# Performance work log

Measured on AMD Instinct MI355X. Metric: run time of the kernel, lower is better.

Reference implementation:

```python
import jax, jax.numpy as jnp
import numpy as np

B, N, IN_C, OUT_C, H, M, E = 1, 20000, 256, 64, 4, 30, 320000
EPS = 1e-6


def _projection_matrix(m, d, seed=0):
    # NodeFormer create_projection_matrix: stacked transposed-QR blocks, rows
    # rescaled by norms of iid gaussian rows (scaling=0).
    rng = np.random.RandomState(seed)
    blocks = []
    nb_full = m // d
    for _ in range(nb_full):
        q, _ = np.linalg.qr(rng.randn(d, d))
        blocks.append(q.T)
    rem = m - nb_full * d
    if rem > 0:
        q, _ = np.linalg.qr(rng.randn(d, d))
        blocks.append(q.T[:rem])
    final = np.vstack(blocks)
    multiplier = np.linalg.norm(rng.randn(m, d), axis=1)
    return jnp.asarray(multiplier[:, None] * final, dtype=jnp.float32)


def _linear(key, out_f, in_f):
    k1, k2 = jax.random.split(key)
    s = 1.0 / np.sqrt(in_f)
    w = jax.random.uniform(k1, (out_f, in_f), jnp.float32, -s, s)
    b = jax.random.uniform(k2, (out_f,), jnp.float32, -s, s)
    return w, b


def setup_inputs() -> dict:
    key = jax.random.key(0)
    ks = jax.random.split(key, 8)
    Wq_w, Wq_b = _linear(ks[3], H * OUT_C, IN_C)
    Wk_w, Wk_b = _linear(ks[4], H * OUT_C, IN_C)
    Wv_w, Wv_b = _linear(ks[5], H * OUT_C, IN_C)
    Wo_w, Wo_b = _linear(ks[6], OUT_C, H * OUT_C)
    return {
        'z': jax.random.normal(ks[0], (B, N, IN_C), jnp.float32),
        'feat': jax.random.normal(ks[1], (B, N, IN_C), jnp.float32),
        'edge_index': jax.random.randint(ks[2], (2, E), 0, N),
        'tau': jnp.asarray(0.25, jnp.float32),
        'Wq_w': Wq_w, 'Wq_b': Wq_b,
        'Wk_w': Wk_w, 'Wk_b': Wk_b,
        'Wv_w': Wv_w, 'Wv_b': Wv_b,
        'Wo_w': Wo_w, 'Wo_b': Wo_b,
        'b_param': jnp.full((1, H), 0.1, jnp.float32),  # rb_order=1, sigmoid init
        'proj': _projection_matrix(M, OUT_C),
    }


def _softmax_kernel(x, proj, is_query):
    # Performer positive softmax kernel feature map. x: [B,N,H,D] -> [B,N,H,M]
    d = x.shape[-1]
    x = x * (float(d) ** -0.25)
    ratio = 1.0 / jnp.sqrt(jnp.asarray(proj.shape[0], x.dtype))
    xd = jnp.einsum('bnhd,md->bnhm', x, proj)
    diag = 0.5 * jnp.sum(x * x, axis=-1, keepdims=True)
    if is_query:
        mx = jnp.max(xd, axis=-1, keepdims=True)
    else:
        mx = jnp.max(jnp.max(xd, axis=-1, keepdims=True), axis=1, keepdims=True)
    return ratio * (jnp.exp(xd - diag - mx) + EPS)


def reference(z, feat, edge_index, tau, Wq_w, Wq_b, Wk_w, Wk_b, Wv_w, Wv_b,
              Wo_w, Wo_b, b_param, proj):
    Bn, Nn = z.shape[0], z.shape[1]
    q = (feat @ Wq_w.T + Wq_b).reshape(Bn, Nn, H, OUT_C)
    k = (feat @ Wk_w.T + Wk_b).reshape(Bn, Nn, H, OUT_C)
    v = (z @ Wv_w.T + Wv_b).reshape(Bn, Nn, H, OUT_C)

    inv = 1.0 / jnp.sqrt(tau)
    qp = _softmax_kernel(q * inv, proj, True)    # [B,N,H,M]
    kp = _softmax_kernel(k * inv, proj, False)   # [B,N,H,M]

    # Linear (kernelized) attention, O(N*H*M*D)
    kvs = jnp.einsum('bnhm,bnhd->bhmd', kp, v)
    num = jnp.einsum('bnhm,bhmd->bnhd', qp, kvs)
    den = jnp.einsum('bnhm,bhm->bnh', qp, jnp.sum(kp, axis=1))[..., None]
    z_next = num / den                            # [B,N,H,D]

    # Relational bias: GCN-style normalized scatter with per-head scalar weight
    row, col = edge_index[0], edge_index[1]
    d_in = jnp.zeros((Nn,), z.dtype).at[col].add(1.0)
    d_out = jnp.zeros((Nn,), z.dtype).at[row].add(1.0)
    edge_w = jnp.nan_to_num(jnp.sqrt(1.0 / d_in[col]) * jnp.sqrt(1.0 / d_out[row]),
                            nan=0.0, posinf=0.0, neginf=0.0)    # [E]
    msgs = v[:, row] * edge_w[None, :, None, None]              # [B,E,H,D]
    agg = jnp.zeros_like(v).at[:, col].add(msgs)                # [B,N,H,D]
    z_next = z_next + jax.nn.sigmoid(b_param[0])[None, None, :, None] * agg

    out = z_next.reshape(Bn, Nn, H * OUT_C) @ Wo_w.T + Wo_b     # [B,N,OUT_C]
    return out
```

## Files before the change

kernel.cpp:

```cpp
#include <hip/hip_runtime.h>

#define NN 20000
#define EE 320000
#define RATIO_F 0.18257418583505536f
#define EPS_F 1e-6f
#define SCALE_D4 0.35355339059327373f
#define NCH 157

typedef _Float16 f16x8 __attribute__((ext_vector_type(8)));
typedef _Float16 f16x4 __attribute__((ext_vector_type(4)));
typedef float f32x4 __attribute__((ext_vector_type(4)));

__device__ __forceinline__ unsigned fenc(float x) {
  unsigned u = __float_as_uint(x);
  return (u & 0x80000000u) ? ~u : (u | 0x80000000u);
}
__device__ __forceinline__ float fdec(unsigned u) {
  return (u & 0x80000000u) ? __uint_as_float(u & 0x7FFFFFFFu) : __uint_as_float(~u);
}
__device__ __forceinline__ void fma4(float* a, float s, float4 b) {
  a[0] = fmaf(s, b.x, a[0]);
  a[1] = fmaf(s, b.y, a[1]);
  a[2] = fmaf(s, b.z, a[2]);
  a[3] = fmaf(s, b.w, a[3]);
}
__device__ __forceinline__ void gload16(const void* g, void* l) {
  __builtin_amdgcn_global_load_lds(
      (const __attribute__((address_space(1))) unsigned int*)g,
      (__attribute__((address_space(3))) unsigned int*)l, 16, 0, 0);
}

__global__ __launch_bounds__(256)
void k0_build(const float* __restrict__ Wq, const float* __restrict__ Wk,
              const float* __restrict__ Wv, const float* __restrict__ bq,
              const float* __restrict__ bk, const float* __restrict__ bv,
              const float* __restrict__ proj, const float* __restrict__ tau,
              const float* __restrict__ Wo, const int* __restrict__ ei,
              const float* __restrict__ feat, const float* __restrict__ zin,
              _Float16* __restrict__ Wf, float* __restrict__ bbig,
              _Float16* __restrict__ WoFh, _Float16* __restrict__ WoFl,
              int* __restrict__ dini, int* __restrict__ douti,
              _Float16* __restrict__ feath, _Float16* __restrict__ zh16) {
  const int blk = blockIdx.x;
  const int i = threadIdx.x;
  if (blk >= 1401) {
    int cb = blk - 1401;
    const float* src;
    _Float16* dst;
    if (cb < 2500) { src = feat; dst = feath; }
    else           { src = zin;  dst = zh16; cb -= 2500; }
    const size_t off = (size_t)cb * 2048 + i * 8;
    const float4 a = *(const float4*)(src + off);
    const float4 b = *(const float4*)(src + off + 4);
    f16x8 o;
    o[0] = (_Float16)a.x; o[1] = (_Float16)a.y;
    o[2] = (_Float16)a.z; o[3] = (_Float16)a.w;
    o[4] = (_Float16)b.x; o[5] = (_Float16)b.y;
    o[6] = (_Float16)b.z; o[7] = (_Float16)b.w;
    *(f16x8*)(dst + off) = o;
    return;
  }
  if (blk >= 1088) {
    const int q = (blk - 1088) * 256 + i;
    if (q < EE / 4) {
      const int4 r4 = *(const int4*)(ei + q * 4);
      const int4 c4 = *(const int4*)(ei + EE + q * 4);
      atomicAdd(&dini[c4.x], 1); atomicAdd(&dini[c4.y], 1);
      atomicAdd(&dini[c4.z], 1); atomicAdd(&dini[c4.w], 1);
      atomicAdd(&douti[r4.x], 1); atomicAdd(&douti[r4.y], 1);
      atomicAdd(&douti[r4.z], 1); atomicAdd(&douti[r4.w], 1);
    }
    return;
  }
  const int kt = i >> 5, gg = (i >> 3) & 3, j = i & 7;
  if (blk >= 1024) {
    const int col = blk - 1024;
    const float val = Wo[col * 256 + i];
    const int lane = gg * 16 + (col & 15);
    const size_t off = (size_t)((col >> 4) * 8 + kt) * 512 + lane * 8 + j;
    const _Float16 hb = (_Float16)val;
    WoFh[off] = hb;
    WoFl[off] = (_Float16)(val - (float)hb);
    return;
  }
  const int col = blk;
  const float s = rsqrtf(tau[0]) * SCALE_D4;
  float val = 0.f, bias = 0.f;
  if (col < 256) {
    val = Wq[col * 256 + i]; bias = bq[col];
  } else if (col < 512) {
    const int c = col - 256;
    val = Wk[c * 256 + i]; bias = bk[c];
  } else if (col < 768) {
    const int c = col - 512;
    val = Wv[c * 256 + i]; bias = bv[c];
  } else {
    const int rr = col - 768;
    const int grp = rr >> 7;
    const int h = (rr >> 5) & 3, m = rr & 31;
    if (m < 30) {
      const float* W = grp ? Wk : Wq;
      const float* bb = grp ? bk : bq;
      float a = 0.f, ba = 0.f;
#pragma unroll 8
      for (int d = 0; d < 64; ++d) {
        const float pr = proj[m * 64 + d];
        a  = fmaf(pr, W[(h * 64 + d) * 256 + i], a);
        ba = fmaf(pr, bb[h * 64 + d], ba);
      }
      val = s * a; bias = s * ba;
    }
  }
  const int lane = gg * 16 + (col & 15);
  const size_t off = (size_t)((col >> 4) * 8 + kt) * 512 + lane * 8 + j;
  Wf[off] = (_Float16)val;
  if (i == 0) bbig[col] = bias;
}

__device__ __forceinline__ int ct_of(int s, int isv, int h, int y) {
  if (isv) return 32 + (y - 4) * 8 + s;
  if (s < 4)  return h * 4 + s;
  if (s < 8)  return 16 + h * 4 + (s - 4);
  if (s < 10) return 48 + 2 * h + (s - 8);
  return 56 + 2 * h + (s - 10);
}

__global__ __launch_bounds__(512, 4)
void k1m(const _Float16* __restrict__ feath, const _Float16* __restrict__ zh16,
         const _Float16* __restrict__ Wf, const float* __restrict__ bbig,
         const float* __restrict__ tau,
         _Float16* __restrict__ qph, _Float16* __restrict__ kbufh,
         _Float16* __restrict__ vh, unsigned* __restrict__ kmaxU,
         const int* __restrict__ ei, const int* __restrict__ coff,
         int* __restrict__ cursor, int* __restrict__ crow,
         const int* __restrict__ douti, float* __restrict__ rw) {
  __shared__ __align__(16) _Float16 blds[12 * 2048];
  const int blk = blockIdx.x;
  const int t = threadIdx.x;
  if (blk >= 1567) {
    const int n = (blk - 1567) * 512 + t;
    if (n < NN) rw[n] = rsqrtf((float)douti[n]);
    return;
  }
  if (blk >= 942) {
    const int e = (blk - 942) * 512 + t;
    const int r = ei[e], c = ei[EE + e];
    const int pos = atomicAdd(&cursor[c], 1);
    crow[coff[c] + pos] = r;
    return;
  }
  const int y = blk / 157;
  const int h = y & 3;
  const int wid = t >> 6, lane = t & 63;
  const int g = lane >> 4, cl = lane & 15;
  const int rbase = (blk - y * 157) * 128 + wid * 16;
  int arow = rbase + cl; if (arow > NN - 1) arow = NN - 1;

  if (y < 4) {
    const _Float16* arp = feath + (size_t)arow * 256;
#pragma unroll
    for (int r = 0; r < 6; ++r) {
      const int idx = r * 4096 + t * 8;
      const int s = idx >> 11, wi = idx & 2047;
      gload16(Wf + (size_t)ct_of(s, 0, h, y) * 4096 + wi, &blds[idx]);
    }
    f16x8 Ah[4];
#pragma unroll
    for (int l = 0; l < 4; ++l)
      Ah[l] = *(const f16x8*)(arp + l * 32 + g * 8);
    __syncthreads();
    f16x8 Ah2[4];
#pragma unroll
    for (int l = 0; l < 4; ++l)
      Ah2[l] = *(const f16x8*)(arp + (l + 4) * 32 + g * 8);
    f32x4 acc[12];
#pragma unroll
    for (int s = 0; s < 12; ++s) acc[s] = (f32x4){0.f, 0.f, 0.f, 0.f};
#pragma unroll
    for (int ktl = 0; ktl < 4; ++ktl) {
#pragma unroll
      for (int s = 0; s < 12; ++s) {
        const f16x8 b = *(const f16x8*)&blds[s * 2048 + ktl * 512 + lane * 8];
        acc[s] = __builtin_amdgcn_mfma_f32_16x16x32_f16(Ah[ktl], b, acc[s], 0, 0, 0);
      }
    }
    __syncthreads();
#pragma unroll
    for (int r = 0; r < 6; ++r) {
      const int idx = r * 4096 + t * 8;
      const int s = idx >> 11, wi = idx & 2047;
      gload16(Wf + (size_t)ct_of(s, 0, h, y) * 4096 + 2048 + wi, &blds[idx]);
    }
    __syncthreads();
#pragma unroll
    for (int ktl = 0; ktl < 4; ++ktl) {
#pragma unroll
      for (int s = 0; s < 12; ++s) {
        const f16x8 b = *(const f16x8*)&blds[s * 2048 + ktl * 512 + lane * 8];
        acc[s] = __builtin_amdgcn_mfma_f32_16x16x32_f16(Ah2[ktl], b, acc[s], 0, 0, 0);
      }
    }
#pragma unroll
    for (int s = 0; s < 12; ++s) {
      const float bb = bbig[ct_of(s, 0, h, y) * 16 + cl];
#pragma unroll
      for (int j = 0; j < 4; ++j) acc[s][j] += bb;
    }
    const float sc = rsqrtf(tau[0]) * SCALE_D4;
    const float h2 = 0.5f * sc * sc;
    float dsq[4], dsk[4];
#pragma unroll
    for (int j = 0; j < 4; ++j) {
      dsq[j] = acc[0][j] * acc[0][j] + acc[1][j] * acc[1][j] +
               acc[2][j] * acc[2][j] + acc[3][j] * acc[3][j];
      dsk[j] = acc[4][j] * acc[4][j] + acc[5][j] * acc[5][j] +
               acc[6][j] * acc[6][j] + acc[7][j] * acc[7][j];
    }
#pragma unroll
    for (int m = 1; m < 16; m <<= 1) {
#pragma unroll
      for (int j = 0; j < 4; ++j) {
        dsq[j] += __shfl_xor(dsq[j], m);
        dsk[j] += __shfl_xor(dsk[j], m);
      }
    }
    {
#pragma unroll
      for (int j = 0; j < 4; ++j) {
        const float x0 = acc[8][j], x1 = acc[9][j];
        float mv = fmaxf(x0, (cl < 14) ? x1 : -3.4e38f);
#pragma unroll
        for (int m = 1; m < 16; m <<= 1) mv = fmaxf(mv, __shfl_xor(mv, m));
        const float dg = h2 * dsq[j];
        const int r = rbase + 4 * g + j;
        if (r < NN) {
          _Float16* dst = qph + (size_t)r * 120 + h * 30;
          dst[cl] = (_Float16)(RATIO_F * (expf(x0 - dg - mv) + EPS_F));
          if (cl < 14)
            dst[16 + cl] = (_Float16)(RATIO_F * (expf(x1 - dg - mv) + EPS_F));
        }
      }
    }
    {
      float wmax = -3.4e38f;
#pragma unroll
      for (int j = 0; j < 4; ++j) {
        const float x0 = acc[10][j], x1 = acc[11][j];
        float mv = fmaxf(x0, (cl < 14) ? x1 : -3.4e38f);
#pragma unroll
        for (int m = 1; m < 16; m <<= 1) mv = fmaxf(mv, __shfl_xor(mv, m));
        wmax = fmaxf(wmax, mv);
        const float dg = h2 * dsk[j];
        const int r = rbase + 4 * g + j;
        if (r < NN) {
          _Float16* dst = kbufh + (size_t)r * 120 + h * 30;
          dst[cl] = (_Float16)(x0 - dg);
          if (cl < 14) dst[16 + cl] = (_Float16)(x1 - dg);
        }
      }
      wmax = fmaxf(wmax, __shfl_xor(wmax, 16));
      wmax = fmaxf(wmax, __shfl_xor(wmax, 32));
      if (lane == 0) atomicMax(&kmaxU[h], fenc(wmax));
    }
  } else {
    const _Float16* arp = zh16 + (size_t)arow * 256;
#pragma unroll
    for (int r = 0; r < 4; ++r) {
      const int idx = r * 4096 + t * 8;
      const int s = idx >> 11, wi = idx & 2047;
      gload16(Wf + (size_t)ct_of(s, 1, h, y) * 4096 + wi, &blds[idx]);
    }
    f16x8 Ah[4];
#pragma unroll
    for (int l = 0; l < 4; ++l)
      Ah[l] = *(const f16x8*)(arp + l * 32 + g * 8);
    __syncthreads();
    f16x8 Ah2[4];
#pragma unroll
    for (int l = 0; l < 4; ++l)
      Ah2[l] = *(const f16x8*)(arp + (l + 4) * 32 + g * 8);
    f32x4 acc[8];
#pragma unroll
    for (int s = 0; s < 8; ++s) acc[s] = (f32x4){0.f, 0.f, 0.f, 0.f};
#pragma unroll
    for (int ktl = 0; ktl < 4; ++ktl) {
#pragma unroll
      for (int s = 0; s < 8; ++s) {
        const f16x8 b = *(const f16x8*)&blds[s * 2048 + ktl * 512 + lane * 8];
        acc[s] = __builtin_amdgcn_mfma_f32_16x16x32_f16(Ah[ktl], b, acc[s], 0, 0, 0);
      }
    }
    __syncthreads();
#pragma unroll
    for (int r = 0; r < 4; ++r) {
      const int idx = r * 4096 + t * 8;
      const int s = idx >> 11, wi = idx & 2047;
      gload16(Wf + (size_t)ct_of(s, 1, h, y) * 4096 + 2048 + wi, &blds[idx]);
    }
    __syncthreads();
#pragma unroll
    for (int ktl = 0; ktl < 4; ++ktl) {
#pragma unroll
      for (int s = 0; s < 8; ++s) {
        const f16x8 b = *(const f16x8*)&blds[s * 2048 + ktl * 512 + lane * 8];
        acc[s] = __builtin_amdgcn_mfma_f32_16x16x32_f16(Ah2[ktl], b, acc[s], 0, 0, 0);
      }
    }
#pragma unroll
    for (int s = 0; s < 8; ++s) {
      const int ct = ct_of(s, 1, h, y);
      const float bb = bbig[ct * 16 + cl];
      const int colb = (ct - 32) * 16 + cl;
#pragma unroll
      for (int j = 0; j < 4; ++j) {
        const int r = rbase + 4 * g + j;
        if (r < NN) vh[(size_t)r * 256 + colb] = (_Float16)(acc[s][j] + bb);
      }
    }
  }
}

__global__ __launch_bounds__(256)
void k3_kvs(const _Float16* __restrict__ kbr, const _Float16* __restrict__ vh,
            const unsigned* __restrict__ kmaxU, float* __restrict__ partial) {
  __shared__ float kpch[128 * 32];
  __shared__ float vch[128 * 68];
  const int h = blockIdx.y;
  const int n0 = blockIdx.x * 128;
  const int cnt = min(128, NN - n0);
  const int t = threadIdx.x;
  const float mx = fdec(kmaxU[h]);
  const int m = t >> 3, dg = t & 7, d0 = dg * 8;
#pragma unroll
  for (int l = 0; l < 15; ++l) {
    const int flat = l * 256 + t;
    const int nl = flat / 30, mm = flat - nl * 30;
    kpch[nl * 32 + mm] = (nl < cnt)
        ? RATIO_F * (expf((float)kbr[(size_t)(n0 + nl) * 120 + h * 30 + mm] - mx) + EPS_F)
        : 0.f;
  }
#pragma unroll
  for (int l = 0; l < 8; ++l) {
    const int f4 = l * 256 + t;
    const int nl = f4 >> 4, dd = (f4 & 15) * 4;
    float4 vv = make_float4(0.f, 0.f, 0.f, 0.f);
    if (nl < cnt) {
      f16x4 u = *(const f16x4*)(vh + (size_t)(n0 + nl) * 256 + h * 64 + dd);
      vv = make_float4((float)u[0], (float)u[1], (float)u[2], (float)u[3]);
    }
    *(float4*)&vch[nl * 68 + dd] = vv;
  }
  __syncthreads();
  float acc[8] = {0, 0, 0, 0, 0, 0, 0, 0};
  float asum = 0.f;
  const int ms = (m < 30) ? m : 0;
  for (int nl = 0; nl < cnt; ++nl) {
    const float kv = kpch[nl * 32 + ms];
    const float4 va = *(const float4*)&vch[nl * 68 + d0];
    const float4 vb = *(const float4*)&vch[nl * 68 + d0 + 4];
    fma4(&acc[0], kv, va);
    fma4(&acc[4], kv, vb);
    asum += kv;
  }
  if (m < 30) {
    float* dst = partial + ((size_t)blockIdx.y * NCH + blockIdx.x) * 1952 + m * 64 + d0;
#pragma unroll
    for (int j = 0; j < 8; ++j) dst[j] = acc[j];
    if (dg == 0)
      partial[((size_t)blockIdx.y * NCH + blockIdx.x) * 1952 + 1920 + m] = asum;
  }
}

__global__ __launch_bounds__(256)
void k7g3b(const int* __restrict__ coff, const int* __restrict__ crow,
           const float* __restrict__ rw, const _Float16* __restrict__ vh,
           _Float16* __restrict__ aggh, const float* __restrict__ partial,
           float* __restrict__ kvs, float* __restrict__ ksum) {
  const int blk = blockIdx.x;
  if (blk >= 5000) {
    const int idx = (blk - 5000) * 256 + threadIdx.x;
    if (idx >= 4 * 1952) return;
    const int h = idx / 1952, q = idx - h * 1952;
    float s = 0.f;
    for (int c = 0; c < NCH; ++c)
      s += partial[((size_t)h * NCH + c) * 1952 + q];
    if (q < 1920) kvs[h * 1920 + q] = s;
    else if (q < 1950) ksum[h * 30 + (q - 1920)] = s;
    return;
  }
  const int node = blk * 4 + (threadIdx.x >> 6);
  const int lane = threadIdx.x & 63;
  const int o0 = coff[node], o1 = coff[node + 1];
  float a0 = 0.f, a1 = 0.f, a2 = 0.f, a3 = 0.f;
  if (o1 > o0) {
    int e = o0;
    for (; e + 16 <= o1; e += 16) {
      int rr[16];
#pragma unroll
      for (int u = 0; u < 16; ++u) rr[u] = crow[e + u];
      float ww[16];
#pragma unroll
      for (int u = 0; u < 16; ++u) ww[u] = rw[rr[u]];
#pragma unroll
      for (int u = 0; u < 16; ++u) {
        const f16x4 vv = *(const f16x4*)(vh + (size_t)rr[u] * 256 + lane * 4);
        a0 = fmaf(ww[u], (float)vv[0], a0);
        a1 = fmaf(ww[u], (float)vv[1], a1);
        a2 = fmaf(ww[u], (float)vv[2], a2);
        a3 = fmaf(ww[u], (float)vv[3], a3);
      }
    }
    for (; e + 4 <= o1; e += 4) {
      int rr[4];
#pragma unroll
      for (int u = 0; u < 4; ++u) rr[u] = crow[e + u];
      float ww[4];
#pragma unroll
      for (int u = 0; u < 4; ++u) ww[u] = rw[rr[u]];
#pragma unroll
      for (int u = 0; u < 4; ++u) {
        const f16x4 vv = *(const f16x4*)(vh + (size_t)rr[u] * 256 + lane * 4);
        a0 = fmaf(ww[u], (float)vv[0], a0);
        a1 = fmaf(ww[u], (float)vv[1], a1);
        a2 = fmaf(ww[u], (float)vv[2], a2);
        a3 = fmaf(ww[u], (float)vv[3], a3);
      }
    }
    for (; e < o1; ++e) {
      const int r = crow[e];
      const float wr = rw[r];
      const f16x4 vv = *(const f16x4*)(vh + (size_t)r * 256 + lane * 4);
      a0 = fmaf(wr, (float)vv[0], a0);
      a1 = fmaf(wr, (float)vv[1], a1);
      a2 = fmaf(wr, (float)vv[2], a2);
      a3 = fmaf(wr, (float)vv[3], a3);
    }
    const float rin = rsqrtf((float)(o1 - o0));
    a0 *= rin; a1 *= rin; a2 *= rin; a3 *= rin;
  }
  f16x4 st;
  st[0] = (_Float16)a0; st[1] = (_Float16)a1;
  st[2] = (_Float16)a2; st[3] = (_Float16)a3;
  *(f16x4*)(aggh + (size_t)node * 256 + lane * 4) = st;
}

__global__ __launch_bounds__(256)
void k4_attn(const _Float16* __restrict__ qph, const float* __restrict__ kvs,
             const float* __restrict__ ksum, const _Float16* __restrict__ aggh,
             const float* __restrict__ bp, _Float16* __restrict__ zh) {
  __shared__ float kvsl[120 * 68];
  __shared__ float ksl[120];
  __shared__ float qpl[32 * 120];
  const int t = threadIdx.x;
  const int n0 = blockIdx.x * 32;
#pragma unroll
  for (int l = 0; l < 30; ++l) {
    const int f = l * 256 + t;
    const int hm = f >> 6, d = f & 63;
    kvsl[hm * 68 + d] = kvs[f];
  }
  if (t < 120) ksl[t] = ksum[t];
#pragma unroll
  for (int l = 0; l < 15; ++l) {
    const int f = l * 256 + t;
    qpl[f] = (float)qph[(size_t)n0 * 120 + f];
  }
  __syncthreads();
  const int nl = t >> 3, dg = t & 7, d0 = dg * 8;
  const float* qrow = &qpl[nl * 120];
  float den[4] = {0, 0, 0, 0};
  for (int m = 0; m < 30; ++m) {
#pragma unroll
    for (int hh = 0; hh < 4; ++hh) den[hh] = fmaf(qrow[hh * 30 + m], ksl[hh * 30 + m], den[hh]);
  }
  float acc[4][8] = {};
  for (int m = 0; m < 30; ++m) {
#pragma unroll
    for (int hh = 0; hh < 4; ++hh) {
      const float qv = qrow[hh * 30 + m];
      const float* kr = &kvsl[(hh * 30 + m) * 68 + d0];
      const float4 ka = *(const float4*)kr;
      const float4 kb = *(const float4*)(kr + 4);
      fma4(&acc[hh][0], qv, ka);
      fma4(&acc[hh][4], qv, kb);
    }
  }
  const size_t n = n0 + nl;
#pragma unroll
  for (int hh = 0; hh < 4; ++hh) {
    const float inv = 1.0f / den[hh];
    const float sg = 1.f / (1.f + expf(-bp[hh]));
    const f16x8 ag = *(const f16x8*)(aggh + n * 256 + hh * 64 + d0);
    f16x8 o;
#pragma unroll
    for (int jj = 0; jj < 8; ++jj)
      o[jj] = (_Float16)(acc[hh][jj] * inv + sg * (float)ag[jj]);
    *(f16x8*)(zh + n * 256 + hh * 64 + d0) = o;
  }
}

__global__ __launch_bounds__(1024)
void k6a_scan(const int* __restrict__ cnt, int* __restrict__ off) {
  __shared__ int s[1024];
  const int t = threadIdx.x;
  int4 v[5];
  int sum = 0;
  const int4* p4 = (const int4*)(cnt + t * 20);
#pragma unroll
  for (int i = 0; i < 5; ++i) {
    v[i] = p4[i];
    sum += v[i].x + v[i].y + v[i].z + v[i].w;
  }
  s[t] = sum;
  __syncthreads();
  for (int o = 1; o < 1024; o <<= 1) {
    const int add = (t >= o) ? s[t - o] : 0;
    __syncthreads();
    s[t] += add;
    __syncthreads();
  }
  int run = (t == 0) ? 0 : s[t - 1];
  if (t == 0) off[0] = 0;
  const int base = t * 20;
#pragma unroll
  for (int i = 0; i < 5; ++i) {
    const int vals[4] = {v[i].x, v[i].y, v[i].z, v[i].w};
#pragma unroll
    for (int j = 0; j < 4; ++j) {
      const int idx = base + i * 4 + j;
      if (idx < NN) { run += vals[j]; off[idx + 1] = run; }
    }
  }
}

__global__ __launch_bounds__(512, 4)
void k8m_out(const _Float16* __restrict__ zh, const _Float16* __restrict__ WoFh,
             const _Float16* __restrict__ WoFl, const float* __restrict__ bo,
             float* __restrict__ out) {
  __shared__ __align__(16) _Float16 blds[8 * 4096];
  const int t = threadIdx.x;
  const int wid = t >> 6, lane = t & 63;
  const int g = lane >> 4, cl = lane & 15;
  const int rt = wid >> 2, ct = wid & 3;
  const int rbase = blockIdx.x * 32 + rt * 16;
  int arow = rbase + cl; if (arow > NN - 1) arow = NN - 1;
#pragma unroll
  for (int s = 0; s < 4; ++s) {
    gload16(WoFh + (size_t)s * 4096 + t * 8, &blds[(s * 512 + t) * 8]);
    gload16(WoFl + (size_t)s * 4096 + t * 8, &blds[((s + 4) * 512 + t) * 8]);
  }
  const _Float16* zr = zh + (size_t)arow * 256;
  f16x8 Ah[8];
#pragma unroll
  for (int kt = 0; kt < 8; ++kt)
    Ah[kt] = *(const f16x8*)(zr + kt * 32 + g * 8);
  __syncthreads();
  f32x4 acc = {0.f, 0.f, 0.f, 0.f};
#pragma unroll
  for (int kt = 0; kt < 8; ++kt) {
    const f16x8 bh = *(const f16x8*)&blds[ct * 4096 + kt * 512 + lane * 8];
    const f16x8 bl = *(const f16x8*)&blds[(ct + 4) * 4096 + kt * 512 + lane * 8];
    acc = __builtin_amdgcn_mfma_f32_16x16x32_f16(Ah[kt], bh, acc, 0, 0, 0);
    acc = __builtin_amdgcn_mfma_f32_16x16x32_f16(Ah[kt], bl, acc, 0, 0, 0);
  }
  const float bb = bo[ct * 16 + cl];
#pragma unroll
  for (int j = 0; j < 4; ++j) {
    const int r = rbase + 4 * g + j;
    if (r < NN) out[(size_t)r * 64 + ct * 16 + cl] = acc[j] + bb;
  }
}

extern "C" void kernel_launch(void* const* d_in, const int* in_sizes, int n_in,
                              void* d_out, int out_size, void* d_ws, size_t ws_size,
                              hipStream_t stream) {
  (void)in_sizes; (void)n_in; (void)out_size; (void)ws_size;
  const float* z    = (const float*)d_in[0];
  const float* feat = (const float*)d_in[1];
  const int*   ei   = (const int*)d_in[2];
  const float* tau  = (const float*)d_in[3];
  const float* Wq_w = (const float*)d_in[4];
  const float* Wq_b = (const float*)d_in[5];
  const float* Wk_w = (const float*)d_in[6];
  const float* Wk_b = (const float*)d_in[7];
  const float* Wv_w = (const float*)d_in[8];
  const float* Wv_b = (const float*)d_in[9];
  const float* Wo_w = (const float*)d_in[10];
  const float* Wo_b = (const float*)d_in[11];
  const float* bp   = (const float*)d_in[12];
  const float* proj = (const float*)d_in[13];
  float* out = (float*)d_out;

  char* p = (char*)d_ws;
  auto alloc = [&](size_t bytes) { char* r = p; p += (bytes + 255) & ~(size_t)255; return r; };
  _Float16* Wf    = (_Float16*)alloc((size_t)256 * 1024 * 2);
  _Float16* WoFh  = (_Float16*)alloc((size_t)64 * 256 * 2);
  _Float16* WoFl  = (_Float16*)alloc((size_t)64 * 256 * 2);
  float*    bbig  = (float*)alloc(1024 * 4);
  _Float16* feath = (_Float16*)alloc((size_t)NN * 256 * 2);
  _Float16* zh16  = (_Float16*)alloc((size_t)NN * 256 * 2);
  _Float16* vh    = (_Float16*)alloc((size_t)NN * 256 * 2);
  _Float16* aggh  = (_Float16*)alloc((size_t)NN * 256 * 2);
  _Float16* qph   = (_Float16*)alloc((size_t)NN * 120 * 2);
  _Float16* kbufh = (_Float16*)alloc((size_t)NN * 120 * 2);
  _Float16* zh    = (_Float16*)alloc((size_t)NN * 256 * 2);
  float*    partial = (float*)alloc((size_t)4 * NCH * 1952 * 4);
  float*    kvs   = (float*)alloc(7680 * 4);
  float*    ksum  = (float*)alloc(120 * 4);
  float*    rw    = (float*)alloc((size_t)NN * 4);
  char* z0 = p;
  unsigned* kmaxU = (unsigned*)alloc(16);
  int*      dini  = (int*)alloc((size_t)20480 * 4);
  int*      douti = (int*)alloc((size_t)NN * 4);
  int*      cursor= (int*)alloc((size_t)NN * 4);
  char* z1 = p;
  int*      coff  = (int*)alloc((size_t)(NN + 1) * 4);
  int*      crow  = (int*)alloc((size_t)EE * 4);

  hipMemsetAsync(z0, 0, (size_t)(z1 - z0), stream);

  k0_build<<<1401 + 5000, 256, 0, stream>>>(
      Wq_w, Wk_w, Wv_w, Wq_b, Wk_b, Wv_b, proj, tau, Wo_w, ei, feat, z,
      Wf, bbig, WoFh, WoFl, dini, douti, feath, zh16);
  k6a_scan<<<1, 1024, 0, stream>>>(dini, coff);
  k1m<<<1607, 512, 0, stream>>>(feath, zh16, Wf, bbig, tau, qph, kbufh, vh,
                                kmaxU, ei, coff, cursor, crow, douti, rw);
  k3_kvs<<<dim3(NCH, 4), 256, 0, stream>>>(kbufh, vh, kmaxU, partial);
  k7g3b<<<5000 + (4 * 1952 + 255) / 256, 256, 0, stream>>>(
      coff, crow, rw, vh, aggh, partial, kvs, ksum);
  k4_attn<<<NN / 32, 256, 0, stream>>>(qph, kvs, ksum, aggh, bp, zh);
  k8m_out<<<628, 512, 0, stream>>>(zh, WoFh, WoFl, Wo_b, out);
}
```

Before: 233.2 us.

## Pack edge weights into CSR records and reduce kvs partials via atomics

During CSR construction each edge now stores its source row together with the precomputed out-degree weight as an int2 record. The gather kernel therefore reads the weight contiguously instead of doing a dependent random lookup into a per-node weight array, and the separate rw pass is removed. The k3_kvs kernel now accumulates its per-chunk results straight into kvs/ksum with float atomics, which removes the partial buffer and the reduction blocks that were folded into the gather kernel. The trade-offs are atomic contention on a small accumulator (4×1950 floats, hit by 157 blocks per head), non-deterministic summation order, and twice the CSR record size.

```diff
diff --git a/kernel.cpp b/kernel.cpp
--- a/kernel.cpp
+++ b/kernel.cpp
@@ -132,21 +132,18 @@
          _Float16* __restrict__ qph, _Float16* __restrict__ kbufh,
          _Float16* __restrict__ vh, unsigned* __restrict__ kmaxU,
          const int* __restrict__ ei, const int* __restrict__ coff,
-         int* __restrict__ cursor, int* __restrict__ crow,
-         const int* __restrict__ douti, float* __restrict__ rw) {
+         int* __restrict__ cursor, int2* __restrict__ crowR,
+         const int* __restrict__ douti) {
   __shared__ __align__(16) _Float16 blds[12 * 2048];
   const int blk = blockIdx.x;
   const int t = threadIdx.x;
-  if (blk >= 1567) {
-    const int n = (blk - 1567) * 512 + t;
-    if (n < NN) rw[n] = rsqrtf((float)douti[n]);
-    return;
-  }
   if (blk >= 942) {
     const int e = (blk - 942) * 512 + t;
     const int r = ei[e], c = ei[EE + e];
+    const float w = rsqrtf((float)douti[r]);
     const int pos = atomicAdd(&cursor[c], 1);
-    crow[coff[c] + pos] = r;
+    int2 rec; rec.x = r; rec.y = __float_as_int(w);
+    crowR[coff[c] + pos] = rec;
     return;
   }
   const int y = blk / 157;
@@ -322,11 +319,13 @@
 
 __global__ __launch_bounds__(256)
 void k3_kvs(const _Float16* __restrict__ kbr, const _Float16* __restrict__ vh,
-            const unsigned* __restrict__ kmaxU, float* __restrict__ partial) {
+            const unsigned* __restrict__ kmaxU, float* __restrict__ kvs,
+            float* __restrict__ ksum) {
   __shared__ float kpch[128 * 32];
   __shared__ float vch[128 * 68];
-  const int h = blockIdx.y;
-  const int n0 = blockIdx.x * 128;
+  const int h = blockIdx.x / NCH;
+  const int cx = blockIdx.x - h * NCH;
+  const int n0 = cx * 128;
   const int cnt = min(128, NN - n0);
   const int t = threadIdx.x;
   const float mx = fdec(kmaxU[h]);
@@ -363,77 +362,58 @@
     asum += kv;
   }
   if (m < 30) {
-    float* dst = partial + ((size_t)blockIdx.y * NCH + blockIdx.x) * 1952 + m * 64 + d0;
-#pragma unroll
-    for (int j = 0; j < 8; ++j) dst[j] = acc[j];
-    if (dg == 0)
-      partial[((size_t)blockIdx.y * NCH + blockIdx.x) * 1952 + 1920 + m] = asum;
+    float* dst = kvs + (size_t)(h * 30 + m) * 64 + d0;
+#pragma unroll
+    for (int j = 0; j < 8; ++j) atomicAdd(dst + j, acc[j]);
+    if (dg == 0) atomicAdd(&ksum[h * 30 + m], asum);
   }
 }
 
 __global__ __launch_bounds__(256)
-void k7g3b(const int* __restrict__ coff, const int* __restrict__ crow,
-           const float* __restrict__ rw, const _Float16* __restrict__ vh,
-           _Float16* __restrict__ aggh, const float* __restrict__ partial,
-           float* __restrict__ kvs, float* __restrict__ ksum) {
-  const int blk = blockIdx.x;
-  if (blk >= 5000) {
-    const int idx = (blk - 5000) * 256 + threadIdx.x;
-    if (idx >= 4 * 1952) return;
-    const int h = idx / 1952, q = idx - h * 1952;
-    float s = 0.f;
-    for (int c = 0; c < NCH; ++c)
-      s += partial[((size_t)h * NCH + c) * 1952 + q];
-    if (q < 1920) kvs[h * 1920 + q] = s;
-    else if (q < 1950) ksum[h * 30 + (q - 1920)] = s;
-    return;
-  }
-  const int node = blk * 4 + (threadIdx.x >> 6);
+void k7g_gather(const int* __restrict__ coff, const int2* __restrict__ crowR,
+                const _Float16* __restrict__ vh, _Float16* __restrict__ aggh) {
+  const int node = blockIdx.x * 4 + (threadIdx.x >> 6);
   const int lane = threadIdx.x & 63;
   const int o0 = coff[node], o1 = coff[node + 1];
   float a0 = 0.f, a1 = 0.f, a2 = 0.f, a3 = 0.f;
   if (o1 > o0) {
     int e = o0;
     for (; e + 16 <= o1; e += 16) {
-      int rr[16];
-#pragma unroll
-      for (int u = 0; u < 16; ++u) rr[u] = crow[e + u];
-      float ww[16];
-#pragma unroll
-      for (int u = 0; u < 16; ++u) ww[u] = rw[rr[u]];
+      int2 rc[16];
+#pragma unroll
+      for (int u = 0; u < 16; ++u) rc[u] = crowR[e + u];
 #pragma unroll
       for (int u = 0; u < 16; ++u) {
-        const f16x4 vv = *(const f16x4*)(vh + (size_t)rr[u] * 256 + lane * 4);
-        a0 = fmaf(ww[u], (float)vv[0], a0);
-        a1 = fmaf(ww[u], (float)vv[1], a1);
-        a2 = fmaf(ww[u], (float)vv[2], a2);
-        a3 = fmaf(ww[u], (float)vv[3], a3);
+        const float w = __int_as_float(rc[u].y);
+        const f16x4 vv = *(const f16x4*)(vh + (size_t)rc[u].x * 256 + lane * 4);
+        a0 = fmaf(w, (float)vv[0], a0);
+        a1 = fmaf(w, (float)vv[1], a1);
+        a2 = fmaf(w, (float)vv[2], a2);
+        a3 = fmaf(w, (float)vv[3], a3);
       }
     }
     for (; e + 4 <= o1; e += 4) {
-      int rr[4];
-#pragma unroll
-      for (int u = 0; u < 4; ++u) rr[u] = crow[e + u];
-      float ww[4];
-#pragma unroll
-      for (int u = 0; u < 4; ++u) ww[u] = rw[rr[u]];
+      int2 rc[4];
+#pragma unroll
+      for (int u = 0; u < 4; ++u) rc[u] = crowR[e + u];
 #pragma unroll
       for (int u = 0; u < 4; ++u) {
-        const f16x4 vv = *(const f16x4*)(vh + (size_t)rr[u] * 256 + lane * 4);
-        a0 = fmaf(ww[u], (float)vv[0], a0);
-        a1 = fmaf(ww[u], (float)vv[1], a1);
-        a2 = fmaf(ww[u], (float)vv[2], a2);
-        a3 = fmaf(ww[u], (float)vv[3], a3);
+        const float w = __int_as_float(rc[u].y);
+        const f16x4 vv = *(const f16x4*)(vh + (size_t)rc[u].x * 256 + lane * 4);
+        a0 = fmaf(w, (float)vv[0], a0);
+        a1 = fmaf(w, (float)vv[1], a1);
+        a2 = fmaf(w, (float)vv[2], a2);
+        a3 = fmaf(w, (float)vv[3], a3);
       }
     }
     for (; e < o1; ++e) {
-      const int r = crow[e];
-      const float wr = rw[r];
-      const f16x4 vv = *(const f16x4*)(vh + (size_t)r * 256 + lane * 4);
-      a0 = fmaf(wr, (float)vv[0], a0);
-      a1 = fmaf(wr, (float)vv[1], a1);
-      a2 = fmaf(wr, (float)vv[2], a2);
-      a3 = fmaf(wr, (float)vv[3], a3);
+      const int2 rc = crowR[e];
+      const float w = __int_as_float(rc.y);
+      const f16x4 vv = *(const f16x4*)(vh + (size_t)rc.x * 256 + lane * 4);
+      a0 = fmaf(w, (float)vv[0], a0);
+      a1 = fmaf(w, (float)vv[1], a1);
+      a2 = fmaf(w, (float)vv[2], a2);
+      a3 = fmaf(w, (float)vv[3], a3);
     }
     const float rin = rsqrtf((float)(o1 - o0));
     a0 *= rin; a1 *= rin; a2 *= rin; a3 *= rin;
@@ -604,18 +584,16 @@
   _Float16* qph   = (_Float16*)alloc((size_t)NN * 120 * 2);
   _Float16* kbufh = (_Float16*)alloc((size_t)NN * 120 * 2);
   _Float16* zh    = (_Float16*)alloc((size_t)NN * 256 * 2);
-  float*    partial = (float*)alloc((size_t)4 * NCH * 1952 * 4);
+  int2*     crowR = (int2*)alloc((size_t)EE * 8);
+  int*      coff  = (int*)alloc((size_t)(NN + 1) * 4);
+  char* z0 = p;
+  unsigned* kmaxU = (unsigned*)alloc(16);
   float*    kvs   = (float*)alloc(7680 * 4);
   float*    ksum  = (float*)alloc(120 * 4);
-  float*    rw    = (float*)alloc((size_t)NN * 4);
-  char* z0 = p;
-  unsigned* kmaxU = (unsigned*)alloc(16);
   int*      dini  = (int*)alloc((size_t)20480 * 4);
   int*      douti = (int*)alloc((size_t)NN * 4);
   int*      cursor= (int*)alloc((size_t)NN * 4);
   char* z1 = p;
-  int*      coff  = (int*)alloc((size_t)(NN + 1) * 4);
-  int*      crow  = (int*)alloc((size_t)EE * 4);
 
   hipMemsetAsync(z0, 0, (size_t)(z1 - z0), stream);
 
@@ -623,11 +601,10 @@
       Wq_w, Wk_w, Wv_w, Wq_b, Wk_b, Wv_b, proj, tau, Wo_w, ei, feat, z,
       Wf, bbig, WoFh, WoFl, dini, douti, feath, zh16);
   k6a_scan<<<1, 1024, 0, stream>>>(dini, coff);
-  k1m<<<1607, 512, 0, stream>>>(feath, zh16, Wf, bbig, tau, qph, kbufh, vh,
-                                kmaxU, ei, coff, cursor, crow, douti, rw);
-  k3_kvs<<<dim3(NCH, 4), 256, 0, stream>>>(kbufh, vh, kmaxU, partial);
-  k7g3b<<<5000 + (4 * 1952 + 255) / 256, 256, 0, stream>>>(
-      coff, crow, rw, vh, aggh, partial, kvs, ksum);
+  k1m<<<1567, 512, 0, stream>>>(feath, zh16, Wf, bbig, tau, qph, kbufh, vh,
+                                kmaxU, ei, coff, cursor, crowR, douti);
+  k3_kvs<<<NCH * 4, 256, 0, stream>>>(kbufh, vh, kmaxU, kvs, ksum);
+  k7g_gather<<<NN / 4, 256, 0, stream>>>(coff, crowR, vh, aggh);
   k4_attn<<<NN / 32, 256, 0, stream>>>(qph, kvs, ksum, aggh, bp, zh);
   k8m_out<<<628, 512, 0, stream>>>(zh, WoFh, WoFl, Wo_b, out);
 }
```

New measurement: 267.0 us. 1.15x slower.
